# Performance work log

Hardware: AMD Instinct MI355X
Metric: run time of the kernel (lower is better)

## Reference

```python
import jax, jax.numpy as jnp
import numpy as np

D_MODEL = 1024
NUM_HEADS = 16
DEPTH = D_MODEL // NUM_HEADS
MAX_LEN = 5000
B, S = 4, 1024


def _dense(x, W, b):
    return x @ W + b


def _split_heads(x, n_heads, depth):
    # [..., S, D] -> [..., H, S, depth]
    *lead, s, d = x.shape
    x = x.reshape(*lead, s, n_heads, depth)
    return jnp.swapaxes(x, -3, -2)


def setup_inputs() -> dict:
    key = jax.random.key(0)
    ks = jax.random.split(key, 12)
    w = 0.02  # glorot-ish scale to keep softmax logits sane
    inp = {
        'q': jax.random.normal(ks[0], (B, S, D_MODEL), jnp.float32),
        'k': jax.random.normal(ks[1], (B, S, D_MODEL), jnp.float32),
        'v': jax.random.normal(ks[2], (B, S, D_MODEL), jnp.float32),
        'Wq': jax.random.normal(ks[3], (D_MODEL, D_MODEL), jnp.float32) * w,
        'bq': jnp.zeros((D_MODEL,), jnp.float32),
        'Wk': jax.random.normal(ks[4], (D_MODEL, D_MODEL), jnp.float32) * w,
        'bk': jnp.zeros((D_MODEL,), jnp.float32),
        'Wv': jax.random.normal(ks[5], (D_MODEL, D_MODEL), jnp.float32) * w,
        'bv': jnp.zeros((D_MODEL,), jnp.float32),
        'Uq': jax.random.normal(ks[6], (D_MODEL, D_MODEL), jnp.float32) * w,
        'buq': jnp.zeros((D_MODEL,), jnp.float32),
        'Uk': jax.random.normal(ks[7], (D_MODEL, D_MODEL), jnp.float32) * w,
        'buk': jnp.zeros((D_MODEL,), jnp.float32),
        'pos_table': jax.random.normal(ks[8], (MAX_LEN, D_MODEL), jnp.float32) * w,
        'theta_cc': jnp.zeros((1, NUM_HEADS, 1, 1), jnp.float32),
        'theta_co': jnp.zeros((1, NUM_HEADS, 1, 1), jnp.float32),
        'theta_oc': jnp.zeros((1, NUM_HEADS, 1, 1), jnp.float32),
        'Wo': jax.random.normal(ks[9], (D_MODEL, D_MODEL), jnp.float32) * w,
        'bo': jnp.zeros((D_MODEL,), jnp.float32),
    }
    return inp


def reference(q, k, v, Wq, bq, Wk, bk, Wv, bv, Uq, buq, Uk, buk,
              pos_table, theta_cc, theta_co, theta_oc, Wo, bo):
    b, s, d = q.shape
    # content projections -> [B,H,S,depth]
    q_c = _split_heads(_dense(q, Wq, bq), NUM_HEADS, DEPTH)
    k_c = _split_heads(_dense(k, Wk, bk), NUM_HEADS, DEPTH)
    v_c = _split_heads(_dense(v, Wv, bv), NUM_HEADS, DEPTH)
    content_scores = jnp.einsum('bhqd,bhkd->bhqk', q_c, k_c)

    # untied positional scores (shared across batch): [1,H,S,S]
    pos_emb = pos_table[:s]                               # [S,D]
    q_p = _split_heads(_dense(pos_emb, Uq, buq)[None], NUM_HEADS, DEPTH)
    k_p = _split_heads(_dense(pos_emb, Uk, buk)[None], NUM_HEADS, DEPTH)
    pos_scores = jnp.einsum('bhqd,bhkd->bhqk', q_p, k_p)  # [1,H,S,S]

    # CLS-row/col overrides with learnable thetas
    pos_scores = pos_scores.at[:, :, 1:, 0:1].set(jnp.broadcast_to(theta_oc, (1, NUM_HEADS, s - 1, 1)))
    pos_scores = pos_scores.at[:, :, 0:1, 1:].set(jnp.broadcast_to(theta_co, (1, NUM_HEADS, 1, s - 1)))
    pos_scores = pos_scores.at[:, :, 0:1, 0:1].set(theta_cc)

    scores = (content_scores + pos_scores) / jnp.sqrt(jnp.float32(DEPTH))
    attn = jax.nn.softmax(scores, axis=-1)
    out = jnp.einsum('bhqk,bhkd->bhqd', attn, v_c)        # [B,H,S,depth]
    out = jnp.swapaxes(out, 1, 2).reshape(b, s, d)        # [B,S,D]
    return _dense(out, Wo, bo)
```

## Files before the change

### kernel.cpp

```cpp
#include <hip/hip_runtime.h>
#include <hip/hip_bf16.h>

typedef __hip_bfloat16 bf16;
typedef unsigned short u16;
typedef __attribute__((ext_vector_type(8))) short short8;
typedef __attribute__((ext_vector_type(4))) float f32x4;

#define D_MODEL 1024
#define NUM_HEADS 16
#define DEPTH 64
#define BATCH 4
#define SEQ 1024
#define BS (BATCH * SEQ)

__device__ __forceinline__ float ldDyn(const void* p, size_t i, int isbf) {
  return isbf ? __bfloat162float(((const bf16*)p)[i]) : ((const float*)p)[i];
}
__device__ __forceinline__ u16 f2bf(float f) {
  bf16 h = __float2bfloat16(f);
  return *(u16*)&h;
}
__device__ __forceinline__ void gl2lds16(const void* g, void* l) {
  __builtin_amdgcn_global_load_lds((const __attribute__((address_space(1))) unsigned int*)g,
                                   (__attribute__((address_space(3))) unsigned int*)l, 16, 0, 0);
}

__global__ void detect_kernel(const u16* __restrict__ q, int* __restrict__ flag) {
  if (threadIdx.x == 0 && blockIdx.x == 0) {
    int sane = 0;
    for (int i = 0; i < 64; ++i) {
      u16 h = q[2 * i];
      int e = (h >> 7) & 0xFF;
      if (e >= 100 && e <= 150) ++sane;
    }
    *flag = (sane >= 48) ? 1 : 0;
  }
}

__global__ __launch_bounds__(256) void transpose_w(
    const void* W0, const void* W1, const void* W2, const void* W3, const void* W4,
    const void* W5, u16* __restrict__ WT, const int* __restrict__ flagp) {
  const int isbf = *flagp;
  const int z = blockIdx.z;
  const void* W = (z == 0) ? W0 : (z == 1) ? W1 : (z == 2) ? W2
                 : (z == 3) ? W3 : (z == 4) ? W4 : W5;
  u16* out = WT + (size_t)z * D_MODEL * D_MODEL;
  __shared__ u16 tile[32][33];
  const int t = threadIdx.x;
  const int tx = t & 31, ty = t >> 5;
  const int r0 = blockIdx.y * 32, c0 = blockIdx.x * 32;
#pragma unroll
  for (int i = 0; i < 4; ++i) {
    size_t gi = (size_t)(r0 + ty + 8 * i) * D_MODEL + c0 + tx;
    tile[ty + 8 * i][tx] = isbf ? ((const u16*)W)[gi] : f2bf(((const float*)W)[gi]);
  }
  __syncthreads();
#pragma unroll
  for (int i = 0; i < 4; ++i)
    out[(size_t)(c0 + ty + 8 * i) * D_MODEL + r0 + tx] = tile[tx][ty + 8 * i];
}

struct GArgs {
  const void* A[5];
  const u16* W[5];
  const void* bias[5];
  void* C[5];
  int Mr[5];
  int om[5];
};

template <int ABF, int GATE>
__global__ __launch_bounds__(256) void gemm_mfma(GArgs ga, const int* __restrict__ flagp) {
  const int isbf = *flagp;
  if (GATE && isbf != ABF) return;
  const int z = blockIdx.z;
  const int M = ga.Mr[z];
  const int lin = blockIdx.x + 8 * blockIdx.y;
  const int xcd = lin & 7;
  const int loc = lin >> 3;
  const int rowb = (loc & 3) * 8 + xcd;
  const int colb = loc >> 2;
  const int row0 = rowb * 128, col0 = colb * 128;
  if (row0 >= M) return;
  const void* A = ga.A[z];
  const u16* WT = ga.W[z];
  const void* bias = ga.bias[z];
  void* C = ga.C[z];
  const int omode = ga.om[z];

  __shared__ short As[2][128][32];
  __shared__ short Bs[2][128][32];
  const int t = threadIdx.x;
  const int wave = t >> 6, lane = t & 63;
  const int quad = lane >> 4, c16 = lane & 15;
  const int wrow = wave >> 1, wcol = wave & 1;

  f32x4 acc[4][4];
#pragma unroll
  for (int mt = 0; mt < 4; ++mt)
#pragma unroll
    for (int nt = 0; nt < 4; ++nt) acc[mt][nt] = {0.f, 0.f, 0.f, 0.f};

#define G_STAGE(K0, BUF)                                                                  \
  {                                                                                       \
    _Pragma("unroll") for (int i = 0; i < 2; ++i) {                                       \
      int L = t + 256 * i;                                                                \
      int r = L >> 2;                                                                     \
      int kc = (L & 3) ^ (r & 3);        \
      gl2lds16(WT + (size_t)(col0 + r) * 1024 + (K0) + kc * 8,                            \
               (char*)&Bs[BUF][0][0] + (size_t)(i * 256 + wave * 64) * 16);               \
      if (ABF) {                                                                          \
        gl2lds16((const u16*)A + (size_t)(row0 + r) * 1024 + (K0) + kc * 8,               \
                 (char*)&As[BUF][0][0] + (size_t)(i * 256 + wave * 64) * 16);             \
      } else {                                                                            \
        const float* af = (const float*)A + (size_t)(row0 + r) * 1024 + (K0) + kc * 8;    \
        float4 lo = *(const float4*)af;                                                   \
        float4 hi = *(const float4*)(af + 4);                                             \
        short8 v;                                                                         \
        u16* pv = (u16*)&v;                                                               \
        pv[0] = f2bf(lo.x); pv[1] = f2bf(lo.y); pv[2] = f2bf(lo.z); pv[3] = f2bf(lo.w);   \
        pv[4] = f2bf(hi.x); pv[5] = f2bf(hi.y); pv[6] = f2bf(hi.z); pv[7] = f2bf(hi.w);   \
        *(short8*)&As[BUF][r][(L & 3) * 8] = v;                                           \
      }                                                                                   \
    }                                                                                     \
  }

  for (int k0 = 0; k0 < 1024; k0 += 64) {
    G_STAGE(k0, 0);
    G_STAGE(k0 + 32, 1);
    __syncthreads();

#pragma unroll
    for (int h = 0; h < 2; ++h) {
      short8 af[4], bfv[4];
#pragma unroll
      for (int mt = 0; mt < 4; ++mt)
        af[mt] = *(const short8*)&As[h][wrow * 64 + mt * 16 + c16][((quad ^ (c16 & 3)) * 8)];
#pragma unroll
      for (int nt = 0; nt < 4; ++nt)
        bfv[nt] = *(const short8*)&Bs[h][wcol * 64 + nt * 16 + c16][((quad ^ (c16 & 3)) * 8)];
#pragma unroll
      for (int nt = 0; nt < 4; ++nt)
#pragma unroll
        for (int mt = 0; mt < 4; ++mt)
          acc[mt][nt] = __builtin_amdgcn_mfma_f32_16x16x32_bf16(af[mt], bfv[nt], acc[mt][nt], 0, 0, 0);
    }
    __syncthreads();
  }
#undef G_STAGE

#pragma unroll
  for (int nt = 0; nt < 4; ++nt) {
    int gc = col0 + wcol * 64 + nt * 16 + c16;
    float bb = ldDyn(bias, gc, isbf);
#pragma unroll
    for (int mt = 0; mt < 4; ++mt) {
      int gr0 = row0 + wrow * 64 + mt * 16 + quad * 4;
      if (omode == 2) {
        __attribute__((ext_vector_type(4))) short pk;
#pragma unroll
        for (int r = 0; r < 4; ++r) pk[r] = (short)f2bf(acc[mt][nt][r] + bb);
        *(__attribute__((ext_vector_type(4))) short*)&((u16*)C)[(size_t)gc * M + gr0] = pk;
      } else if (omode == 1 || isbf) {
#pragma unroll
        for (int r = 0; r < 4; ++r)
          ((bf16*)C)[(size_t)(gr0 + r) * 1024 + gc] = __float2bfloat16(acc[mt][nt][r] + bb);
      } else {
#pragma unroll
        for (int r = 0; r < 4; ++r)
          ((float*)C)[(size_t)(gr0 + r) * 1024 + gc] = acc[mt][nt][r] + bb;
      }
    }
  }
}

__global__ __launch_bounds__(256) void flash_attn(
    const bf16* __restrict__ Qc, const bf16* __restrict__ Kc, const bf16* __restrict__ VcT,
    const bf16* __restrict__ Qp, const bf16* __restrict__ Kp,
    const void* __restrict__ th_cc, const void* __restrict__ th_co,
    const void* __restrict__ th_oc, bf16* __restrict__ O, const int* __restrict__ flagp) {
  const int isbf = *flagp;
  const int h = blockIdx.x, b = blockIdx.y, qt = blockIdx.z;
  const int t = threadIdx.x, wave = t >> 6, lane = t & 63;
  const int quad = lane >> 4, c16 = lane & 15;

  __shared__ short Kt[2][64][128];
  __shared__ short Vt[2][64][64];
  __shared__ short Pt[4][16][64];

  const float tcc = ldDyn(th_cc, h, isbf);
  const float tco = ldDyn(th_co, h, isbf);
  const float toc = ldDyn(th_oc, h, isbf);

  const bf16* kcb = Kc + (size_t)b * SEQ * 1024 + h * 64;
  const bf16* kpb = Kp + h * 64;
  const bf16* vtb = VcT + (size_t)(h * 64) * BS + (size_t)b * SEQ;

  const int rwK = lane >> 4, kcK = lane & 15;
  const int rwV = lane >> 3, kcV = lane & 7;

#define STAGE_K(KT2, BUF)                                                              \
  {                                                                                    \
    _Pragma("unroll") for (int i = 0; i < 4; ++i) {                                    \
      int r = wave * 16 + i * 4 + rwK;                                                 \
      int c = kcK ^ (r & 15);                                                          \
      int key = (KT2)*64 + r;                                                          \
      const bf16* src = (c < 8) ? kcb + (size_t)key * 1024 + c * 8                     \
                                : kpb + (size_t)key * 1024 + c * 8 - 64;               \
      gl2lds16(src, &Kt[BUF][wave * 16 + i * 4][0]);                                   \
    }                                                                                  \
  }
#define STAGE_V(KT2, BUF)                                                              \
  {                                                                                    \
    _Pragma("unroll") for (int j = 0; j < 2; ++j) {                                    \
      int d = wave * 16 + j * 8 + rwV;                                                 \
      int c = kcV ^ (d & 7);                                                           \
      gl2lds16(vtb + (size_t)d * BS + (KT2)*64 + c * 8, &Vt[BUF][wave * 16 + j * 8][0]); \
    }                                                                                  \
  }

  short8 qf[2][4];
#pragma unroll
  for (int mt = 0; mt < 2; ++mt) {
    int qrow = qt * 128 + wave * 32 + mt * 16 + c16;
#pragma unroll
    for (int ks = 0; ks < 4; ++ks) {
      int d = ks * 32 + quad * 8;
      const bf16* src = (d < 64) ? Qc + ((size_t)(b * SEQ + qrow)) * 1024 + h * 64 + d
                                 : Qp + (size_t)qrow * 1024 + h * 64 + (d - 64);
      qf[mt][ks] = *(const short8*)src;
    }
    if (qrow == 0) {
      qf[mt][2] = (short8)0;
      qf[mt][3] = (short8)0;
    }
  }

  f32x4 accO[2][4];
#pragma unroll
  for (int mt = 0; mt < 2; ++mt)
#pragma unroll
    for (int nt = 0; nt < 4; ++nt) accO[mt][nt] = {0.f, 0.f, 0.f, 0.f};
  float lrow[2][4] = {{0.f, 0.f, 0.f, 0.f}, {0.f, 0.f, 0.f, 0.f}};

  STAGE_K(0, 0);
  STAGE_V(0, 0);
  __syncthreads();
  if (t < 8) *(short8*)&Kt[0][0][64 + t * 8] = (short8)0;
  __syncthreads();

  for (int kt = 0; kt < 16; ++kt) {
    const int cur = kt & 1, nxt = cur ^ 1;
    if (kt < 15) {
      STAGE_K(kt + 1, nxt);
      STAGE_V(kt + 1, nxt);
    }

    f32x4 accS[2][4];
#pragma unroll
    for (int mt = 0; mt < 2; ++mt)
#pragma unroll
      for (int nt = 0; nt < 4; ++nt) accS[mt][nt] = {0.f, 0.f, 0.f, 0.f};
#pragma unroll
    for (int nt = 0; nt < 4; ++nt)
#pragma unroll
      for (int ks = 0; ks < 4; ++ks) {
        short8 kf = *(const short8*)&Kt[cur][nt * 16 + c16][((ks * 4 + quad) ^ c16) * 8];
#pragma unroll
        for (int mt = 0; mt < 2; ++mt)
          accS[mt][nt] = __builtin_amdgcn_mfma_f32_16x16x32_bf16(qf[mt][ks], kf, accS[mt][nt], 0, 0, 0);
      }

    short8 vbreg[2][4];
#pragma unroll
    for (int ks2 = 0; ks2 < 2; ++ks2)
#pragma unroll
      for (int nt = 0; nt < 4; ++nt)
        vbreg[ks2][nt] =
            *(const short8*)&Vt[cur][nt * 16 + c16][(((ks2 * 4 + quad) ^ (c16 & 7)) & 7) * 8];

#pragma unroll
    for (int mt = 0; mt < 2; ++mt) {
      float s[4][4];
#pragma unroll
      for (int nt = 0; nt < 4; ++nt)
#pragma unroll
        for (int r = 0; r < 4; ++r) s[nt][r] = accS[mt][nt][r] * 0.125f;

      if (kt == 0 || (qt == 0 && wave == 0 && mt == 0)) {
#pragma unroll
        for (int nt = 0; nt < 4; ++nt)
#pragma unroll
          for (int r = 0; r < 4; ++r) {
            int kcol = kt * 64 + nt * 16 + c16;
            int qrow = qt * 128 + wave * 32 + mt * 16 + quad * 4 + r;
            float add = 0.f;
            if (qrow == 0 && kcol == 0) add = tcc;
            else if (qrow == 0) add = tco;
            else if (kcol == 0) add = toc;
            s[nt][r] += add * 0.125f;
          }
      }
#pragma unroll
      for (int nt = 0; nt < 4; ++nt)
#pragma unroll
        for (int r = 0; r < 4; ++r) {
          float p = __expf(s[nt][r]);
          lrow[mt][r] += p;
          int row = quad * 4 + r;
          int ch = nt * 2 + (c16 >> 3);
          Pt[wave][row][((ch ^ (row & 7)) * 8) + (c16 & 7)] = (short)f2bf(p);
        }
#pragma unroll
      for (int ks2 = 0; ks2 < 2; ++ks2) {
        short8 pf = *(const short8*)&Pt[wave][c16][(((ks2 * 4 + quad) ^ (c16 & 7)) & 7) * 8];
#pragma unroll
        for (int nt = 0; nt < 4; ++nt)
          accO[mt][nt] = __builtin_amdgcn_mfma_f32_16x16x32_bf16(pf, vbreg[ks2][nt], accO[mt][nt], 0, 0, 0);
      }
    }
    __syncthreads();
  }

#pragma unroll
  for (int d = 1; d < 16; d <<= 1)
#pragma unroll
    for (int mt = 0; mt < 2; ++mt)
#pragma unroll
      for (int r = 0; r < 4; ++r) lrow[mt][r] += __shfl_xor(lrow[mt][r], d, 64);

#pragma unroll
  for (int mt = 0; mt < 2; ++mt)
#pragma unroll
    for (int nt = 0; nt < 4; ++nt)
#pragma unroll
      for (int r = 0; r < 4; ++r) {
        int qrow = qt * 128 + wave * 32 + mt * 16 + quad * 4 + r;
        O[((size_t)(b * SEQ + qrow)) * 1024 + h * 64 + nt * 16 + c16] =
            __float2bfloat16(accO[mt][nt][r] / lrow[mt][r]);
      }
#undef STAGE_K
#undef STAGE_V
}

extern "C" void kernel_launch(void* const* d_in, const int* in_sizes, int n_in,
                              void* d_out, int out_size, void* d_ws, size_t ws_size,
                              hipStream_t stream) {
  const void* q = d_in[0];
  const void* k = d_in[1];
  const void* v = d_in[2];
  const void* Wq = d_in[3];
  const void* bq = d_in[4];
  const void* Wk = d_in[5];
  const void* bk = d_in[6];
  const void* Wv = d_in[7];
  const void* bv = d_in[8];
  const void* Uq = d_in[9];
  const void* buq = d_in[10];
  const void* Uk = d_in[11];
  const void* buk = d_in[12];
  const void* pos = d_in[13];
  const void* th_cc = d_in[14];
  const void* th_co = d_in[15];
  const void* th_oc = d_in[16];
  const void* Wo = d_in[17];
  const void* bo = d_in[18];

  const int M = BS;
  const size_t DD = (size_t)D_MODEL * D_MODEL;
  char* wsb = (char*)d_ws;
  int* flag = (int*)wsb;
  bf16* Qc = (bf16*)(wsb + 256);
  bf16* Kc = Qc + (size_t)M * D_MODEL;
  bf16* VcT = Kc + (size_t)M * D_MODEL;
  bf16* Qp = VcT + (size_t)M * D_MODEL;
  bf16* Kp = Qp + (size_t)SEQ * D_MODEL;
  u16* WT = (u16*)(Kp + (size_t)SEQ * D_MODEL);
  bf16* AO = (bf16*)WT;

  detect_kernel<<<1, 64, 0, stream>>>((const u16*)q, flag);

  dim3 blk(256);
  transpose_w<<<dim3(32, 32, 6), blk, 0, stream>>>(Wq, Wk, Wv, Uq, Uk, Wo, WT, flag);

  GArgs g1 = {{q, k, v, pos, pos},
              {WT + 0 * DD, WT + 1 * DD, WT + 2 * DD, WT + 3 * DD, WT + 4 * DD},
              {bq, bk, bv, buq, buk},
              {Qc, Kc, VcT, Qp, Kp},
              {M, M, M, SEQ, SEQ},
              {1, 1, 2, 1, 1}};
  gemm_mfma<1, 1><<<dim3(8, 32, 5), blk, 0, stream>>>(g1, flag);
  gemm_mfma<0, 1><<<dim3(8, 32, 5), blk, 0, stream>>>(g1, flag);

  flash_attn<<<dim3(NUM_HEADS, BATCH, SEQ / 128), blk, 0, stream>>>(
      Qc, Kc, VcT, Qp, Kp, th_cc, th_co, th_oc, AO, flag);

  GArgs g2 = {{AO, AO, AO, AO, AO},
              {WT + 5 * DD, WT + 5 * DD, WT + 5 * DD, WT + 5 * DD, WT + 5 * DD},
              {bo, bo, bo, bo, bo},
              {d_out, d_out, d_out, d_out, d_out},
              {M, M, M, M, M},
              {0, 0, 0, 0, 0}};
  gemm_mfma<1, 0><<<dim3(8, 32, 1), blk, 0, stream>>>(g2, flag);
}
```

Measured before the change: 288.8 us.

## Pre-convert fp32 inputs to bf16 and double-buffer GEMM K-loop

Adds a separate kernel that converts q/k/v/pos to bf16 once, so the projection GEMM can always use async global-to-LDS loads instead of converting fp32 inside its load stage. The GEMM K-loop becomes a one-stage-ahead double-buffered pipeline with one barrier per 32-wide K step, and the LDS swizzle changes to reduce bank conflicts. The cost is an extra pass over the inputs, plus extra workspace, and the template gating with its duplicate launch goes away.

```diff
diff --git a/kernel.cpp b/kernel.cpp
--- a/kernel.cpp
+++ b/kernel.cpp
@@ -34,6 +34,30 @@
       if (e >= 100 && e <= 150) ++sane;
     }
     *flag = (sane >= 48) ? 1 : 0;
+  }
+}
+
+__global__ __launch_bounds__(256) void convert_in(
+    const void* __restrict__ q, const void* __restrict__ k, const void* __restrict__ v,
+    const void* __restrict__ pos, u16* __restrict__ Qb, u16* __restrict__ Kb,
+    u16* __restrict__ Vb, u16* __restrict__ Pb, const int* __restrict__ flagp) {
+  const int isbf = *flagp;
+  const int z = blockIdx.z;
+  const void* src = (z == 0) ? q : (z == 1) ? k : (z == 2) ? v : pos;
+  u16* dst = (z == 0) ? Qb : (z == 1) ? Kb : (z == 2) ? Vb : Pb;
+  const size_t n8 = ((z == 3) ? (size_t)SEQ * D_MODEL : (size_t)BS * D_MODEL) / 8;
+  for (size_t i = (size_t)blockIdx.x * 256 + threadIdx.x; i < n8; i += (size_t)gridDim.x * 256) {
+    short8 o;
+    if (isbf) {
+      o = ((const short8*)src)[i];
+    } else {
+      const float4* f = (const float4*)src + 2 * i;
+      float4 lo = f[0], hi = f[1];
+      u16* pv = (u16*)&o;
+      pv[0] = f2bf(lo.x); pv[1] = f2bf(lo.y); pv[2] = f2bf(lo.z); pv[3] = f2bf(lo.w);
+      pv[4] = f2bf(hi.x); pv[5] = f2bf(hi.y); pv[6] = f2bf(hi.z); pv[7] = f2bf(hi.w);
+    }
+    ((short8*)dst)[i] = o;
   }
 }
 
@@ -61,7 +85,7 @@
 }
 
 struct GArgs {
-  const void* A[5];
+  const u16* A[5];
   const u16* W[5];
   const void* bias[5];
   void* C[5];
@@ -69,10 +93,8 @@
   int om[5];
 };
 
-template <int ABF, int GATE>
 __global__ __launch_bounds__(256) void gemm_mfma(GArgs ga, const int* __restrict__ flagp) {
   const int isbf = *flagp;
-  if (GATE && isbf != ABF) return;
   const int z = blockIdx.z;
   const int M = ga.Mr[z];
   const int lin = blockIdx.x + 8 * blockIdx.y;
@@ -82,7 +104,7 @@
   const int colb = loc >> 2;
   const int row0 = rowb * 128, col0 = colb * 128;
   if (row0 >= M) return;
-  const void* A = ga.A[z];
+  const u16* A = ga.A[z];
   const u16* WT = ga.W[z];
   const void* bias = ga.bias[z];
   void* C = ga.C[z];
@@ -106,45 +128,36 @@
     _Pragma("unroll") for (int i = 0; i < 2; ++i) {                                       \
       int L = t + 256 * i;                                                                \
       int r = L >> 2;                                                                     \
-      int kc = (L & 3) ^ (r & 3);        \
+      int kc = (L & 3) ^ ((r + (r >> 2)) & 3);                                            \
       gl2lds16(WT + (size_t)(col0 + r) * 1024 + (K0) + kc * 8,                            \
                (char*)&Bs[BUF][0][0] + (size_t)(i * 256 + wave * 64) * 16);               \
-      if (ABF) {                                                                          \
-        gl2lds16((const u16*)A + (size_t)(row0 + r) * 1024 + (K0) + kc * 8,               \
-                 (char*)&As[BUF][0][0] + (size_t)(i * 256 + wave * 64) * 16);             \
-      } else {                                                                            \
-        const float* af = (const float*)A + (size_t)(row0 + r) * 1024 + (K0) + kc * 8;    \
-        float4 lo = *(const float4*)af;                                                   \
-        float4 hi = *(const float4*)(af + 4);                                             \
-        short8 v;                                                                         \
-        u16* pv = (u16*)&v;                                                               \
-        pv[0] = f2bf(lo.x); pv[1] = f2bf(lo.y); pv[2] = f2bf(lo.z); pv[3] = f2bf(lo.w);   \
-        pv[4] = f2bf(hi.x); pv[5] = f2bf(hi.y); pv[6] = f2bf(hi.z); pv[7] = f2bf(hi.w);   \
-        *(short8*)&As[BUF][r][(L & 3) * 8] = v;                                           \
-      }                                                                                   \
+      gl2lds16(A + (size_t)(row0 + r) * 1024 + (K0) + kc * 8,                             \
+               (char*)&As[BUF][0][0] + (size_t)(i * 256 + wave * 64) * 16);               \
     }                                                                                     \
   }
 
-  for (int k0 = 0; k0 < 1024; k0 += 64) {
-    G_STAGE(k0, 0);
-    G_STAGE(k0 + 32, 1);
-    __syncthreads();
-
-#pragma unroll
-    for (int h = 0; h < 2; ++h) {
-      short8 af[4], bfv[4];
+  G_STAGE(0, 0);
+  __syncthreads();
+
+  const int fsw = (c16 + (c16 >> 2)) & 3;
+
+  for (int kk = 0; kk < 32; ++kk) {
+    const int cur = kk & 1;
+    if (kk < 31) G_STAGE((kk + 1) * 32, cur ^ 1);
+
+    short8 af[4], bfv[4];
+#pragma unroll
+    for (int mt = 0; mt < 4; ++mt)
+      af[mt] = *(const short8*)&As[cur][wrow * 64 + mt * 16 + c16][((quad ^ fsw) * 8)];
+#pragma unroll
+    for (int nt = 0; nt < 4; ++nt)
+      bfv[nt] = *(const short8*)&Bs[cur][wcol * 64 + nt * 16 + c16][((quad ^ fsw) * 8)];
+#pragma unroll
+    for (int nt = 0; nt < 4; ++nt)
 #pragma unroll
       for (int mt = 0; mt < 4; ++mt)
-        af[mt] = *(const short8*)&As[h][wrow * 64 + mt * 16 + c16][((quad ^ (c16 & 3)) * 8)];
-#pragma unroll
-      for (int nt = 0; nt < 4; ++nt)
-        bfv[nt] = *(const short8*)&Bs[h][wcol * 64 + nt * 16 + c16][((quad ^ (c16 & 3)) * 8)];
-#pragma unroll
-      for (int nt = 0; nt < 4; ++nt)
-#pragma unroll
-        for (int mt = 0; mt < 4; ++mt)
-          acc[mt][nt] = __builtin_amdgcn_mfma_f32_16x16x32_bf16(af[mt], bfv[nt], acc[mt][nt], 0, 0, 0);
-    }
+        acc[mt][nt] = __builtin_amdgcn_mfma_f32_16x16x32_bf16(af[mt], bfv[nt], acc[mt][nt], 0, 0, 0);
+
     __syncthreads();
   }
 #undef G_STAGE
@@ -377,29 +390,33 @@
   bf16* Kp = Qp + (size_t)SEQ * D_MODEL;
   u16* WT = (u16*)(Kp + (size_t)SEQ * D_MODEL);
   bf16* AO = (bf16*)WT;
+  u16* Qb = WT + 6 * DD;
+  u16* Kb = Qb + (size_t)M * D_MODEL;
+  u16* Vb = Kb + (size_t)M * D_MODEL;
+  u16* Pb = Vb + (size_t)M * D_MODEL;
 
   detect_kernel<<<1, 64, 0, stream>>>((const u16*)q, flag);
 
   dim3 blk(256);
+  convert_in<<<dim3(512, 1, 4), blk, 0, stream>>>(q, k, v, pos, Qb, Kb, Vb, Pb, flag);
   transpose_w<<<dim3(32, 32, 6), blk, 0, stream>>>(Wq, Wk, Wv, Uq, Uk, Wo, WT, flag);
 
-  GArgs g1 = {{q, k, v, pos, pos},
+  GArgs g1 = {{Qb, Kb, Vb, Pb, Pb},
               {WT + 0 * DD, WT + 1 * DD, WT + 2 * DD, WT + 3 * DD, WT + 4 * DD},
               {bq, bk, bv, buq, buk},
               {Qc, Kc, VcT, Qp, Kp},
               {M, M, M, SEQ, SEQ},
               {1, 1, 2, 1, 1}};
-  gemm_mfma<1, 1><<<dim3(8, 32, 5), blk, 0, stream>>>(g1, flag);
-  gemm_mfma<0, 1><<<dim3(8, 32, 5), blk, 0, stream>>>(g1, flag);
+  gemm_mfma<<<dim3(8, 32, 5), blk, 0, stream>>>(g1, flag);
 
   flash_attn<<<dim3(NUM_HEADS, BATCH, SEQ / 128), blk, 0, stream>>>(
       Qc, Kc, VcT, Qp, Kp, th_cc, th_co, th_oc, AO, flag);
 
-  GArgs g2 = {{AO, AO, AO, AO, AO},
+  GArgs g2 = {{(const u16*)AO, (const u16*)AO, (const u16*)AO, (const u16*)AO, (const u16*)AO},
               {WT + 5 * DD, WT + 5 * DD, WT + 5 * DD, WT + 5 * DD, WT + 5 * DD},
               {bo, bo, bo, bo, bo},
               {d_out, d_out, d_out, d_out, d_out},
               {M, M, M, M, M},
               {0, 0, 0, 0, 0}};
-  gemm_mfma<1, 0><<<dim3(8, 32, 1), blk, 0, stream>>>(g2, flag);
-}
+  gemm_mfma<<<dim3(8, 32, 1), blk, 0, stream>>>(g2, flag);
+}
```

New measurement: 291.3 us. About the same (+0.9%).
